# Kernel tuning notes

Measured on AMD Instinct MI355X. Metric: run time of the kernel, lower is better.

Reference implementation:

```python
import jax, jax.numpy as jnp
import numpy as np

T, B, I, H, O = 512, 64, 1024, 1024, 1024
SIGMA = 0.01

def setup_inputs() -> dict:
    key = jax.random.key(0)
    ks = jax.random.split(key, 8)
    return {
        "X": jax.random.normal(ks[0], (T, B, I), dtype=jnp.float32),
        "W_xr": jax.random.normal(ks[1], (I, H), dtype=jnp.float32) * SIGMA,
        "W_xu": jax.random.normal(ks[2], (I, H), dtype=jnp.float32) * SIGMA,
        "W_xh": jax.random.normal(ks[3], (I, H), dtype=jnp.float32) * SIGMA,
        "W_hr": jax.random.normal(ks[4], (H, H), dtype=jnp.float32) * SIGMA,
        "W_hu": jax.random.normal(ks[5], (H, H), dtype=jnp.float32) * SIGMA,
        "W_hh": jax.random.normal(ks[6], (H, H), dtype=jnp.float32) * SIGMA,
        "b_r": jnp.zeros((H,), dtype=jnp.float32),
        "b_u": jnp.zeros((H,), dtype=jnp.float32),
        "b_h": jnp.zeros((H,), dtype=jnp.float32),
        "W_hq": jax.random.normal(ks[7], (H, O), dtype=jnp.float32) * SIGMA,
        "b_q": jnp.zeros((O,), dtype=jnp.float32),
    }

def reference(X, W_xr, W_xu, W_xh, W_hr, W_hu, W_hh, b_r, b_u, b_h, W_hq, b_q):
    # Precompute all input projections in one big batched GEMM: [T,B,3H]
    Xr = X @ W_xr + b_r
    Xu = X @ W_xu + b_u
    Xh = X @ W_xh + b_h

    def step(state, xs):
        xr, xu, xh = xs  # each [B,H]
        R = jax.nn.sigmoid(xr + state @ W_hr)
        U = jax.nn.sigmoid(xu + state @ W_hu)
        Hc = jnp.tanh(xh + (state * R) @ W_hh)
        new_state = U * state + (1.0 - U) * Hc
        return new_state, new_state

    state0 = jnp.zeros((X.shape[1], W_xh.shape[1]), dtype=X.dtype)
    _, states = jax.lax.scan(step, state0, (Xr, Xu, Xh))  # states: [T,B,H]
    outputs = states @ W_hq + b_q  # [T,B,O]
    return outputs, states
```

## Files before the change

### kernel.cpp

```cpp
#include <hip/hip_runtime.h>
#include <stdint.h>

typedef unsigned short u16;
typedef __attribute__((ext_vector_type(8))) short bf16x8;
typedef __attribute__((ext_vector_type(4))) float f32x4;

#define T_STEPS 512
#define BATCH   64
#define HID     1024
#define NWG_SCAN 64

__device__ __forceinline__ u16 f2bf(float f) {
  union { float f; uint32_t u; } v; v.f = f;
  uint32_t r = (v.u + 0x7fffu + ((v.u >> 16) & 1u)) >> 16;
  return (u16)r;
}
__device__ __forceinline__ float bf2f(u16 h) {
  union { uint32_t u; float f; } v; v.u = ((uint32_t)h) << 16;
  return v.f;
}
__device__ __forceinline__ float sigmoidf_(float x) {
  return 1.0f / (1.0f + __expf(-x));
}
__device__ __forceinline__ float fast_tanhf(float x) {
  float xc = fminf(15.f, fmaxf(-15.f, x));
  float e = __expf(2.f * xc);
  return (e - 1.f) / (e + 1.f);
}

__device__ __forceinline__ void store_bf16_sc1(u16* p, u16 v) {
  uint32_t vv = v;
  asm volatile("global_store_short %0, %1, off sc1" :: "v"(p), "v"(vv) : "memory");
}

__global__ __launch_bounds__(256) void transpose_cast(const float* __restrict__ src,
                                                      u16* __restrict__ dst) {
  __shared__ float tile[32][33];
  int bx = blockIdx.x * 32;
  int by = blockIdx.y * 32;
  for (int i = threadIdx.y; i < 32; i += 8)
    tile[i][threadIdx.x] = src[(size_t)(bx + i) * 1024 + by + threadIdx.x];
  __syncthreads();
  for (int i = threadIdx.y; i < 32; i += 8)
    dst[(size_t)(by + i) * 1024 + bx + threadIdx.x] = f2bf(tile[threadIdx.x][i]);
}

__global__ void concat_bias(const float* __restrict__ br, const float* __restrict__ bu,
                            const float* __restrict__ bh, float* __restrict__ b3) {
  int i = blockIdx.x * blockDim.x + threadIdx.x;
  float v = (i < 1024) ? br[i] : (i < 2048 ? bu[i - 1024] : bh[i - 2048]);
  b3[i] = v;
}

template <int A_F32, int OUT_BF16>
__global__ __launch_bounds__(256) void gemm_bt(const void* __restrict__ Av,
                                               const u16* __restrict__ BT,
                                               const float* __restrict__ bias,
                                               void* __restrict__ Cv,
                                               int M, int N, int K) {
  __shared__ u16 Asm[4096];
  __shared__ u16 Bsm[4096];
  const int tid = threadIdx.x;
  const int lane = tid & 63;
  const int wv = tid >> 6;
  const int wm = wv >> 1, wn = wv & 1;
  const int m0 = blockIdx.x * 128;
  const int n0 = blockIdx.y * 128;

  f32x4 acc[4][4];
#pragma unroll
  for (int i = 0; i < 4; i++)
#pragma unroll
    for (int j = 0; j < 4; j++) acc[i][j] = (f32x4){0.f, 0.f, 0.f, 0.f};

  for (int kt = 0; kt < K; kt += 32) {
    __syncthreads();
#pragma unroll
    for (int i = 0; i < 2; i++) {
      int q = tid + i * 256;
      int m = q >> 2, s = q & 3;
      int bb = s ^ ((m & 3) ^ ((m >> 2) & 3));
      if (A_F32) {
        const float* srcp = (const float*)Av + (size_t)(m0 + m) * K + kt + bb * 8;
        bf16x8 o;
#pragma unroll
        for (int e = 0; e < 8; e++) o[e] = (short)f2bf(srcp[e]);
        *(bf16x8*)&Asm[q * 8] = o;
      } else {
        const u16* srcp = (const u16*)Av + (size_t)(m0 + m) * K + kt + bb * 8;
        *(bf16x8*)&Asm[q * 8] = *(const bf16x8*)srcp;
      }
      const u16* srcb = BT + (size_t)(n0 + m) * K + kt + bb * 8;
      *(bf16x8*)&Bsm[q * 8] = *(const bf16x8*)srcb;
    }
    __syncthreads();

    bf16x8 af[4], bfr[4];
    int bb = lane >> 4;
#pragma unroll
    for (int mt = 0; mt < 4; mt++) {
      int m = wm * 64 + mt * 16 + (lane & 15);
      int s = bb ^ ((m & 3) ^ ((m >> 2) & 3));
      af[mt] = *(const bf16x8*)&Asm[m * 32 + s * 8];
    }
#pragma unroll
    for (int nt = 0; nt < 4; nt++) {
      int n = wn * 64 + nt * 16 + (lane & 15);
      int s = bb ^ ((n & 3) ^ ((n >> 2) & 3));
      bfr[nt] = *(const bf16x8*)&Bsm[n * 32 + s * 8];
    }
#pragma unroll
    for (int mt = 0; mt < 4; mt++)
#pragma unroll
      for (int nt = 0; nt < 4; nt++)
        acc[mt][nt] = __builtin_amdgcn_mfma_f32_16x16x32_bf16(af[mt], bfr[nt], acc[mt][nt], 0, 0, 0);
  }

#pragma unroll
  for (int nt = 0; nt < 4; nt++) {
    int col = n0 + wn * 64 + nt * 16 + (lane & 15);
    float bv = bias[col];
#pragma unroll
    for (int mt = 0; mt < 4; mt++) {
#pragma unroll
      for (int r = 0; r < 4; r++) {
        int row = m0 + wm * 64 + mt * 16 + (lane >> 4) * 4 + r;
        float v = acc[mt][nt][r] + bv;
        if (OUT_BF16)
          ((u16*)Cv)[(size_t)row * N + col] = f2bf(v);
        else
          ((float*)Cv)[(size_t)row * N + col] = v;
      }
    }
  }
}

__global__ __launch_bounds__(256, 1) void gru_scan(const float* __restrict__ W_hr,
                                                   const float* __restrict__ W_hu,
                                                   const float* __restrict__ W_hh,
                                                   u16* __restrict__ Xproj,
                                                   u16* __restrict__ SB,
                                                   float* __restrict__ out_states,
                                                   unsigned* __restrict__ flags) {
  __shared__ u16 lds[49152];
  const int tid = threadIdx.x;
  const int lane = tid & 63;
  const int wv = tid >> 6;
  const int wg = blockIdx.x;

  {
    const int cbase = wg * 16;
#pragma unroll
    for (int s = 0; s < 3; s++) {
      const float* Wsrc = (s == 0) ? W_hr : (s == 1) ? W_hu : W_hh;
      for (int idx = tid; idx < 16384; idx += 256) {
        int kin = idx & 31, nl_ = (idx >> 5) & 15, kb = idx >> 9;
        float v = Wsrc[(size_t)(kb * 32 + kin) * 1024 + cbase + nl_];
        int slot_ = (kin >> 3) ^ (nl_ & 3) ^ ((nl_ >> 2) & 3);
        lds[s * 16384 + ((kb * 16 + nl_) * 4 + slot_) * 8 + (kin & 7)] = f2bf(v);
      }
    }
  }
  __syncthreads();

  unsigned phase = 0;
  const int bb = lane >> 4;
  const int nl = lane & 15;
  const int quad = lane >> 4;
  const int slot = bb ^ ((nl & 3) ^ ((nl >> 2) & 3));
  const int rt = wv;
  const int j = wg * 16 + nl;

  float Ureg[4];
  float Sreg[4] = {0.f, 0.f, 0.f, 0.f};

  float xr[4], xu[4];
  u16* xaddr[4];
  {
    u16* A2_0 = Xproj;
#pragma unroll
    for (int r = 0; r < 4; r++) {
      int b_ = rt * 16 + quad * 4 + r;
      xaddr[r] = A2_0 + (size_t)b_ * 3072 + j;
      xr[r] = bf2f(*xaddr[r]);
      xu[r] = bf2f(Xproj[(size_t)b_ * 3072 + 1024 + j]);
    }
  }

  for (int t = 0; t < T_STEPS; t++) {
    const u16* SBt = SB + (size_t)t * BATCH * HID;
    u16* A2 = Xproj + (size_t)t * 64 * 3072;

    {
      const u16* abase = SBt + (size_t)(rt * 16 + nl) * HID + bb * 8;
      bf16x8 af[32];
#pragma unroll
      for (int kb = 0; kb < 32; kb++) af[kb] = *(const bf16x8*)(abase + kb * 32);

      f32x4 ar0 = (f32x4){0.f, 0.f, 0.f, 0.f}, ar1 = ar0, au0 = ar0, au1 = ar0;
      const u16* lbr = &lds[(nl * 4 + slot) * 8];
#pragma unroll
      for (int kb = 0; kb < 32; kb += 2) {
        bf16x8 br0 = *(const bf16x8*)(lbr + kb * 512);
        bf16x8 bu0 = *(const bf16x8*)(lbr + 16384 + kb * 512);
        bf16x8 br1 = *(const bf16x8*)(lbr + (kb + 1) * 512);
        bf16x8 bu1 = *(const bf16x8*)(lbr + 16384 + (kb + 1) * 512);
        ar0 = __builtin_amdgcn_mfma_f32_16x16x32_bf16(af[kb], br0, ar0, 0, 0, 0);
        au0 = __builtin_amdgcn_mfma_f32_16x16x32_bf16(af[kb], bu0, au0, 0, 0, 0);
        ar1 = __builtin_amdgcn_mfma_f32_16x16x32_bf16(af[kb + 1], br1, ar1, 0, 0, 0);
        au1 = __builtin_amdgcn_mfma_f32_16x16x32_bf16(af[kb + 1], bu1, au1, 0, 0, 0);
      }
      f32x4 accr = ar0 + ar1;
      f32x4 accu = au0 + au1;

#pragma unroll
      for (int r = 0; r < 4; r++) {
        float R = sigmoidf_(accr[r] + xr[r]);
        store_bf16_sc1(xaddr[r], f2bf(R * Sreg[r]));
        Ureg[r] = sigmoidf_(accu[r] + xu[r]);
      }
    }

    asm volatile("s_waitcnt vmcnt(0)" ::: "memory");
    __syncthreads();
    phase++;
    if (tid == 0)
      __hip_atomic_store(&flags[wg], phase, __ATOMIC_RELAXED, __HIP_MEMORY_SCOPE_AGENT);
    float xh[4];
#pragma unroll
    for (int r = 0; r < 4; r++) {
      int b_ = rt * 16 + quad * 4 + r;
      xh[r] = bf2f(Xproj[(size_t)(t * 64 + b_) * 3072 + 2048 + j]);
    }
    if (wv == 0) {
      while (true) {
        unsigned v = __hip_atomic_load(&flags[lane], __ATOMIC_RELAXED, __HIP_MEMORY_SCOPE_AGENT);
        if (__all((int)(v >= phase))) break;
        __builtin_amdgcn_s_sleep(1);
      }
    }
    __syncthreads();
    asm volatile("" ::: "memory");

    {
      const u16* a2base = A2 + (size_t)(rt * 16 + nl) * 3072 + bb * 8;
      bf16x8 af[32];
#pragma unroll
      for (int kb = 0; kb < 32; kb++) af[kb] = *(const bf16x8*)(a2base + kb * 32);

      f32x4 ah0 = (f32x4){0.f, 0.f, 0.f, 0.f}, ah1 = ah0;
      const u16* lbh = &lds[32768 + (nl * 4 + slot) * 8];
#pragma unroll
      for (int kb = 0; kb < 32; kb += 2) {
        bf16x8 bh0 = *(const bf16x8*)(lbh + kb * 512);
        bf16x8 bh1 = *(const bf16x8*)(lbh + (kb + 1) * 512);
        ah0 = __builtin_amdgcn_mfma_f32_16x16x32_bf16(af[kb], bh0, ah0, 0, 0, 0);
        ah1 = __builtin_amdgcn_mfma_f32_16x16x32_bf16(af[kb + 1], bh1, ah1, 0, 0, 0);
      }
      f32x4 acch = ah0 + ah1;

      u16* SBn = SB + (size_t)(t + 1) * BATCH * HID;
#pragma unroll
      for (int r = 0; r < 4; r++) {
        int b_ = rt * 16 + quad * 4 + r;
        float hc = fast_tanhf(acch[r] + xh[r]);
        float snew = Ureg[r] * Sreg[r] + (1.f - Ureg[r]) * hc;
        Sreg[r] = snew;
        store_bf16_sc1(SBn + (size_t)b_ * HID + j, f2bf(snew));
      }
    }

    asm volatile("s_waitcnt vmcnt(0)" ::: "memory");
    __syncthreads();
    phase++;
    if (tid == 0)
      __hip_atomic_store(&flags[wg], phase, __ATOMIC_RELAXED, __HIP_MEMORY_SCOPE_AGENT);
#pragma unroll
    for (int r = 0; r < 4; r++) {
      int b_ = rt * 16 + quad * 4 + r;
      float* p = out_states + (size_t)(t * 64 + b_) * HID + j;
      float v = Sreg[r];
      asm volatile("global_store_dword %0, %1, off" :: "v"(p), "v"(v) : "memory");
    }
    if (t + 1 < T_STEPS) {
      u16* A2n = Xproj + (size_t)(t + 1) * 64 * 3072;
#pragma unroll
      for (int r = 0; r < 4; r++) {
        int b_ = rt * 16 + quad * 4 + r;
        xaddr[r] = A2n + (size_t)b_ * 3072 + j;
        xr[r] = bf2f(*xaddr[r]);
        xu[r] = bf2f(Xproj[(size_t)((t + 1) * 64 + b_) * 3072 + 1024 + j]);
      }
    }
    if (wv == 0) {
      while (true) {
        unsigned v = __hip_atomic_load(&flags[lane], __ATOMIC_RELAXED, __HIP_MEMORY_SCOPE_AGENT);
        if (__all((int)(v >= phase))) break;
        __builtin_amdgcn_s_sleep(1);
      }
    }
    __syncthreads();
    asm volatile("" ::: "memory");
  }
}

extern "C" void kernel_launch(void* const* d_in, const int* in_sizes, int n_in,
                              void* d_out, int out_size, void* d_ws, size_t ws_size,
                              hipStream_t stream) {
  const float* X    = (const float*)d_in[0];
  const float* W_xr = (const float*)d_in[1];
  const float* W_xu = (const float*)d_in[2];
  const float* W_xh = (const float*)d_in[3];
  const float* W_hr = (const float*)d_in[4];
  const float* W_hu = (const float*)d_in[5];
  const float* W_hh = (const float*)d_in[6];
  const float* b_r  = (const float*)d_in[7];
  const float* b_u  = (const float*)d_in[8];
  const float* b_h  = (const float*)d_in[9];
  const float* W_hq = (const float*)d_in[10];
  const float* b_q  = (const float*)d_in[11];

  char* ws = (char*)d_ws;
  size_t off = 0;
  auto alloc = [&](size_t bytes) {
    char* p = ws + off;
    off = (off + bytes + 255) & ~(size_t)255;
    return p;
  };
  u16*      WxT   = (u16*)alloc(3072ull * 1024 * 2);
  u16*      WhqT  = (u16*)alloc(1024ull * 1024 * 2);
  float*    bias3 = (float*)alloc(3072ull * 4);
  u16*      Xproj = (u16*)alloc(32768ull * 3072 * 2);
  u16*      SB    = (u16*)alloc(513ull * BATCH * HID * 2);
  unsigned* flags = (unsigned*)alloc(256);

  hipMemsetAsync(SB, 0, (size_t)BATCH * HID * 2, stream);
  hipMemsetAsync(flags, 0, 256, stream);

  dim3 tb(32, 8);
  dim3 tg(32, 32);
  transpose_cast<<<tg, tb, 0, stream>>>(W_xr, WxT);
  transpose_cast<<<tg, tb, 0, stream>>>(W_xu, WxT + 1024ull * 1024);
  transpose_cast<<<tg, tb, 0, stream>>>(W_xh, WxT + 2048ull * 1024);
  transpose_cast<<<tg, tb, 0, stream>>>(W_hq, WhqT);
  concat_bias<<<12, 256, 0, stream>>>(b_r, b_u, b_h, bias3);

  gemm_bt<1, 1><<<dim3(256, 24), 256, 0, stream>>>(X, WxT, bias3, Xproj, 32768, 3072, 1024);

  float* out_states = (float*)d_out + 33554432ull;
  gru_scan<<<NWG_SCAN, 256, 0, stream>>>(W_hr, W_hu, W_hh, Xproj, SB, out_states, flags);

  gemm_bt<0, 0><<<dim3(256, 8), 256, 0, stream>>>(SB + (size_t)BATCH * HID, WhqT, b_q,
                                                  d_out, 32768, 1024, 1024);
}
```

Baseline: 6.743 ms.

## Replace block-wide grid barriers with per-wave flags and fine-grained readiness polling

The GRU scan used to run two workgroup-wide barriers per half-step, gated on a single flag per workgroup. It now keeps one flag per (wave row, workgroup), so each wave waits only on the 64 producers of its own batch rows and drops __syncthreads. Each 16-byte A-fragment load is issued as soon as the two workgroups that wrote those K columns have set their flags, so loading overlaps with waiting. This adds more atomic polling traffic and inline-asm loads with explicit cache bits, and it relies on relaxed atomics for correct ordering.

```diff
diff --git a/kernel.cpp b/kernel.cpp
--- a/kernel.cpp
+++ b/kernel.cpp
@@ -163,40 +163,52 @@
   }
   __syncthreads();
 
-  unsigned phase = 0;
   const int bb = lane >> 4;
   const int nl = lane & 15;
-  const int quad = lane >> 4;
+  const int quad = bb;
   const int slot = bb ^ ((nl & 3) ^ ((nl >> 2) & 3));
   const int rt = wv;
   const int j = wg * 16 + nl;
+  unsigned* flagrow = flags + rt * 64;
+  unsigned* myflag = flagrow + wg;
 
   float Ureg[4];
   float Sreg[4] = {0.f, 0.f, 0.f, 0.f};
 
   float xr[4], xu[4];
   u16* xaddr[4];
-  {
-    u16* A2_0 = Xproj;
-#pragma unroll
-    for (int r = 0; r < 4; r++) {
-      int b_ = rt * 16 + quad * 4 + r;
-      xaddr[r] = A2_0 + (size_t)b_ * 3072 + j;
-      xr[r] = bf2f(*xaddr[r]);
-      xu[r] = bf2f(Xproj[(size_t)b_ * 3072 + 1024 + j]);
-    }
-  }
+#pragma unroll
+  for (int r = 0; r < 4; r++) {
+    int b_ = rt * 16 + quad * 4 + r;
+    xaddr[r] = Xproj + (size_t)b_ * 3072 + j;
+    xr[r] = bf2f(*xaddr[r]);
+    xu[r] = bf2f(Xproj[(size_t)b_ * 3072 + 1024 + j]);
+  }
+
+  bf16x8 af[32];
 
   for (int t = 0; t < T_STEPS; t++) {
     const u16* SBt = SB + (size_t)t * BATCH * HID;
     u16* A2 = Xproj + (size_t)t * 64 * 3072;
 
     {
+      const unsigned tgt = 2u * (unsigned)t;
       const u16* abase = SBt + (size_t)(rt * 16 + nl) * HID + bb * 8;
-      bf16x8 af[32];
-#pragma unroll
-      for (int kb = 0; kb < 32; kb++) af[kb] = *(const bf16x8*)(abase + kb * 32);
-
+      uint64_t rdy = 0;
+#pragma unroll
+      for (int kb = 0; kb < 32; kb++) {
+        while (((rdy >> (2 * kb)) & 3ull) != 3ull) {
+          unsigned v = __hip_atomic_load(&flagrow[lane], __ATOMIC_RELAXED, __HIP_MEMORY_SCOPE_AGENT);
+          rdy = __ballot((int)(v >= tgt));
+          if (((rdy >> (2 * kb)) & 3ull) != 3ull) __builtin_amdgcn_s_sleep(1);
+        }
+        asm volatile("global_load_dwordx4 %0, %1, off"
+                     : "=v"(af[kb]) : "v"(abase + (size_t)kb * 32) : "memory");
+      }
+      asm volatile("s_waitcnt vmcnt(0)" ::: "memory");
+      __builtin_amdgcn_sched_barrier(0);
+    }
+    {
       f32x4 ar0 = (f32x4){0.f, 0.f, 0.f, 0.f}, ar1 = ar0, au0 = ar0, au1 = ar0;
       const u16* lbr = &lds[(nl * 4 + slot) * 8];
 #pragma unroll
@@ -220,34 +232,34 @@
         Ureg[r] = sigmoidf_(accu[r] + xu[r]);
       }
     }
-
     asm volatile("s_waitcnt vmcnt(0)" ::: "memory");
-    __syncthreads();
-    phase++;
-    if (tid == 0)
-      __hip_atomic_store(&flags[wg], phase, __ATOMIC_RELAXED, __HIP_MEMORY_SCOPE_AGENT);
+    if (lane == 0)
+      __hip_atomic_store(myflag, 2u * (unsigned)t + 1u, __ATOMIC_RELAXED, __HIP_MEMORY_SCOPE_AGENT);
     float xh[4];
 #pragma unroll
     for (int r = 0; r < 4; r++) {
       int b_ = rt * 16 + quad * 4 + r;
       xh[r] = bf2f(Xproj[(size_t)(t * 64 + b_) * 3072 + 2048 + j]);
     }
-    if (wv == 0) {
-      while (true) {
-        unsigned v = __hip_atomic_load(&flags[lane], __ATOMIC_RELAXED, __HIP_MEMORY_SCOPE_AGENT);
-        if (__all((int)(v >= phase))) break;
-        __builtin_amdgcn_s_sleep(1);
-      }
-    }
-    __syncthreads();
-    asm volatile("" ::: "memory");
 
     {
+      const unsigned tgt = 2u * (unsigned)t + 1u;
       const u16* a2base = A2 + (size_t)(rt * 16 + nl) * 3072 + bb * 8;
-      bf16x8 af[32];
-#pragma unroll
-      for (int kb = 0; kb < 32; kb++) af[kb] = *(const bf16x8*)(a2base + kb * 32);
-
+      uint64_t rdy = 0;
+#pragma unroll
+      for (int kb = 0; kb < 32; kb++) {
+        while (((rdy >> (2 * kb)) & 3ull) != 3ull) {
+          unsigned v = __hip_atomic_load(&flagrow[lane], __ATOMIC_RELAXED, __HIP_MEMORY_SCOPE_AGENT);
+          rdy = __ballot((int)(v >= tgt));
+          if (((rdy >> (2 * kb)) & 3ull) != 3ull) __builtin_amdgcn_s_sleep(1);
+        }
+        asm volatile("global_load_dwordx4 %0, %1, off sc0 sc1"
+                     : "=v"(af[kb]) : "v"(a2base + (size_t)kb * 32) : "memory");
+      }
+      asm volatile("s_waitcnt vmcnt(0)" ::: "memory");
+      __builtin_amdgcn_sched_barrier(0);
+    }
+    {
       f32x4 ah0 = (f32x4){0.f, 0.f, 0.f, 0.f}, ah1 = ah0;
       const u16* lbh = &lds[32768 + (nl * 4 + slot) * 8];
 #pragma unroll
@@ -269,12 +281,9 @@
         store_bf16_sc1(SBn + (size_t)b_ * HID + j, f2bf(snew));
       }
     }
-
     asm volatile("s_waitcnt vmcnt(0)" ::: "memory");
-    __syncthreads();
-    phase++;
-    if (tid == 0)
-      __hip_atomic_store(&flags[wg], phase, __ATOMIC_RELAXED, __HIP_MEMORY_SCOPE_AGENT);
+    if (lane == 0)
+      __hip_atomic_store(myflag, 2u * (unsigned)t + 2u, __ATOMIC_RELAXED, __HIP_MEMORY_SCOPE_AGENT);
 #pragma unroll
     for (int r = 0; r < 4; r++) {
       int b_ = rt * 16 + quad * 4 + r;
@@ -292,15 +301,6 @@
         xu[r] = bf2f(Xproj[(size_t)((t + 1) * 64 + b_) * 3072 + 1024 + j]);
       }
     }
-    if (wv == 0) {
-      while (true) {
-        unsigned v = __hip_atomic_load(&flags[lane], __ATOMIC_RELAXED, __HIP_MEMORY_SCOPE_AGENT);
-        if (__all((int)(v >= phase))) break;
-        __builtin_amdgcn_s_sleep(1);
-      }
-    }
-    __syncthreads();
-    asm volatile("" ::: "memory");
   }
 }
 
@@ -332,10 +332,10 @@
   float*    bias3 = (float*)alloc(3072ull * 4);
   u16*      Xproj = (u16*)alloc(32768ull * 3072 * 2);
   u16*      SB    = (u16*)alloc(513ull * BATCH * HID * 2);
-  unsigned* flags = (unsigned*)alloc(256);
+  unsigned* flags = (unsigned*)alloc(1024);
 
   hipMemsetAsync(SB, 0, (size_t)BATCH * HID * 2, stream);
-  hipMemsetAsync(flags, 0, 256, stream);
+  hipMemsetAsync(flags, 0, 1024, stream);
 
   dim3 tb(32, 8);
   dim3 tg(32, 32);
```

Result: slower. 8.019 ms (+18.9%).
